# Optimization experiments

Hardware: AMD Instinct MI355X
Metric: run time of the kernel (lower is better)

## Reference

```python
import jax, jax.numpy as jnp
import numpy as np

T, D, H, E, K = 4096, 1024, 2048, 8, 2  # tokens, model dim, expert hidden, n_experts, top_k
AUX_COEF = 0.01


def setup_inputs() -> dict:
    key = jax.random.key(0)
    ks = jax.random.split(key, 8)
    sd = lambda fan_in: 1.0 / np.sqrt(fan_in)
    x = jax.random.normal(ks[0], (T, D), jnp.float32)
    Wr = jax.random.normal(ks[1], (E, D), jnp.float32) * sd(D)      # router (no bias)
    w1 = jax.random.normal(ks[2], (E, H, D), jnp.float32) * sd(D)   # stacked up-proj
    w2 = jax.random.normal(ks[3], (E, D, H), jnp.float32) * sd(H)   # stacked down-proj
    w3 = jax.random.normal(ks[4], (E, H, D), jnp.float32) * sd(D)   # stacked gate-proj
    w1s = jax.random.normal(ks[5], (H, D), jnp.float32) * sd(D)     # shared expert
    w2s = jax.random.normal(ks[6], (D, H), jnp.float32) * sd(H)
    w3s = jax.random.normal(ks[7], (H, D), jnp.float32) * sd(D)
    return dict(x=x, Wr=Wr, w1=w1, w2=w2, w3=w3, w1s=w1s, w2s=w2s, w3s=w3s)


def _gelu(v):
    return jax.nn.gelu(v, approximate=False)  # torch F.gelu default = exact erf


def reference(x, Wr, w1, w2, w3, w1s, w2s, w3s):
    n_tok = x.shape[0]
    router_out = x @ Wr.T                                   # [T, E]
    router_probs = jax.nn.softmax(router_out, axis=-1)
    _, topk_idx = jax.lax.top_k(router_out, K)              # [T, K]
    topk_probs, _ = jax.lax.top_k(router_probs, K)          # top-k of probs (same order)

    # auxiliary load-balance loss (first-choice density * mean prob)
    expert_mask = jax.nn.one_hot(topk_idx[:, 0], E, dtype=jnp.float32)
    density = expert_mask.mean(axis=0)
    aux_loss = AUX_COEF * jnp.sum(density * router_probs.mean(axis=0)) * E

    # combine weights C[t, e] = sum of routed probs for expert e at token t
    C = jnp.zeros((n_tok, E), x.dtype).at[
        jnp.arange(n_tok)[:, None], topk_idx
    ].add(topk_probs)

    # dense per-expert SwiGLU-style FFN, combined by C (equal math to
    # sort-based dispatch + scatter_add in the original)
    h = _gelu(jnp.einsum('td,ehd->teh', x, w1)) * jnp.einsum('td,ehd->teh', x, w3)
    ye = jnp.einsum('teh,edh->ted', h, w2)                  # [T, E, D]
    out = jnp.einsum('ted,te->td', ye, C)

    # shared expert (always active)
    out = out + (_gelu(x @ w1s.T) * (x @ w3s.T)) @ w2s.T
    return out, aux_loss
```

## Files before the change

kernel.cpp:

```cpp
#include <hip/hip_runtime.h>
#include <hip/hip_bf16.h>
#include <cstdint>

#define T_TOK 4096
#define DMODEL 1024
#define HDIM 2048

typedef short bf16x8 __attribute__((ext_vector_type(8)));
typedef float f32x4 __attribute__((ext_vector_type(4)));
typedef uint32_t u32x4 __attribute__((ext_vector_type(4)));

#define WAITVM(N) asm volatile("s_waitcnt vmcnt(" #N ")" ::: "memory")
#define BARX() asm volatile("s_barrier" ::: "memory")

__device__ __forceinline__ uint32_t cvt_pk_bf16(float lo, float hi) {
  uint32_t d;
  asm("v_cvt_pk_bf16_f32 %0, %1, %2" : "=v"(d) : "v"(lo), "v"(hi));
  return d;
}
__device__ __forceinline__ unsigned short f2bf(float f) {
  uint32_t d;
  asm("v_cvt_pk_bf16_f32 %0, %1, %1" : "=v"(d) : "v"(f));
  return (unsigned short)d;
}
__device__ __forceinline__ float gelu_fast(float v) {
  float z = v * 0.70710678118654752f;
  float az = fabsf(z);
  float t = __frcp_rn(1.0f + 0.3275911f * az);
  float poly = ((((1.061405429f * t - 1.453152027f) * t + 1.421413741f) * t
                 - 0.284496736f) * t + 0.254829592f) * t;
  float er = 1.0f - poly * __expf(-z * z);
  er = (z < 0.f) ? -er : er;
  return 0.5f * v * (1.0f + er);
}
__device__ __forceinline__ void gload16(const void* g, void* lds) {
  __builtin_amdgcn_global_load_lds((const __attribute__((address_space(1))) void*)g,
                                   (__attribute__((address_space(3))) void*)lds, 16, 0, 0);
}
__device__ __forceinline__ u32x4 pk8(const float* s) {
  float4 v0 = ((const float4*)s)[0], v1 = ((const float4*)s)[1];
  u32x4 p = {cvt_pk_bf16(v0.x, v0.y), cvt_pk_bf16(v0.z, v0.w),
             cvt_pk_bf16(v1.x, v1.y), cvt_pk_bf16(v1.z, v1.w)};
  return p;
}

__global__ __launch_bounds__(256) void convert_w(
    const float* __restrict__ w1, const float* __restrict__ w3,
    const float* __restrict__ w1s, const float* __restrict__ w3s,
    const float* __restrict__ w2, const float* __restrict__ w2s,
    short* __restrict__ wB, short* __restrict__ wd) {
  int bid = blockIdx.x;
  if (bid < 18432) {
    int id = bid * 256 + threadIdx.x;
    int e = id >> 19, rem = id & 524287;
    int nf = rem >> 11, k32 = (rem >> 6) & 31, ln = rem & 63;
    int h = (nf >> 1) * 16 + (ln & 15);
    size_t so = (size_t)h * DMODEL + k32 * 32 + (ln >> 4) * 8;
    const float* src = (nf & 1)
        ? ((e < 8) ? w3 + (size_t)e * 2097152 + so : w3s + so)
        : ((e < 8) ? w1 + (size_t)e * 2097152 + so : w1s + so);
    *(u32x4*)(wB + (size_t)id * 8) = pk8(src);
  } else {
    int id = (bid - 18432) * 256 + threadIdx.x;
    int e = id >> 18, rem = id & 262143;
    int d16 = rem >> 12, h32 = (rem >> 6) & 63, ln = rem & 63;
    size_t so = (size_t)(d16 * 16 + (ln & 15)) * HDIM + h32 * 32 + (ln >> 4) * 8;
    const float* s2 = (e < 8) ? w2 + (size_t)e * 2097152 + so : w2s + so;
    *(u32x4*)(wd + (size_t)id * 8) = pk8(s2);
  }
}

__global__ __launch_bounds__(256) void router_kernel(
    const float* __restrict__ x, const float* __restrict__ Wr,
    int* __restrict__ cursor, int* __restrict__ cnt1,
    float* __restrict__ psum, int* __restrict__ perm,
    int* __restrict__ tokpos, float* __restrict__ wtok,
    short* __restrict__ xb) {
  __shared__ float4 sW[8 * 256];
  __shared__ float sP[8];
  int tid = threadIdx.x;
  const float4* W4 = (const float4*)Wr;
  for (int i = tid; i < 2048; i += 256) sW[i] = W4[i];
  if (tid < 8) sP[tid] = 0.f;
  __syncthreads();

  int lane = tid & 63, wid = tid >> 6;
  int t = blockIdx.x * 4 + wid;
  float acc[8] = {0.f, 0.f, 0.f, 0.f, 0.f, 0.f, 0.f, 0.f};
  const float4* x4 = (const float4*)(x + (size_t)t * DMODEL);
#pragma unroll
  for (int it = 0; it < 4; ++it) {
    float4 xv = x4[it * 64 + lane];
    uint2 pk = {cvt_pk_bf16(xv.x, xv.y), cvt_pk_bf16(xv.z, xv.w)};
    *(uint2*)(xb + (size_t)t * DMODEL + it * 256 + lane * 4) = pk;
#pragma unroll
    for (int e = 0; e < 8; ++e) {
      float4 wv = sW[e * 256 + it * 64 + lane];
      acc[e] += xv.x * wv.x + xv.y * wv.y + xv.z * wv.z + xv.w * wv.w;
    }
  }
#pragma unroll
  for (int e = 0; e < 8; ++e)
    for (int off = 32; off; off >>= 1) acc[e] += __shfl_xor(acc[e], off);

  float mx = acc[0];
#pragma unroll
  for (int e = 1; e < 8; ++e) mx = fmaxf(mx, acc[e]);
  float ex[8], s = 0.f;
#pragma unroll
  for (int e = 0; e < 8; ++e) { ex[e] = expf(acc[e] - mx); s += ex[e]; }
  float inv = 1.f / s;
  int e0 = 0;
#pragma unroll
  for (int e = 1; e < 8; ++e) if (acc[e] > acc[e0]) e0 = e;
  int e1 = (e0 == 0) ? 1 : 0;
#pragma unroll
  for (int e = 0; e < 8; ++e) if (e != e0 && acc[e] > acc[e1]) e1 = e;

  if (lane == 0) {
#pragma unroll
    for (int e = 0; e < 8; ++e) atomicAdd(&sP[e], ex[e] * inv);
    atomicAdd(&cnt1[e0], 1);
    int s0 = atomicAdd(&cursor[e0], 1);
    perm[e0 * 4096 + s0] = t;
    int s1 = atomicAdd(&cursor[e1], 1);
    perm[e1 * 4096 + s1] = t;
    tokpos[2 * t] = (e0 << 12) | s0;
    tokpos[2 * t + 1] = (e1 << 12) | s1;
    wtok[2 * t] = ex[e0] * inv;
    wtok[2 * t + 1] = ex[e1] * inv;
  }
  __syncthreads();
  if (tid < 8) atomicAdd(&psum[tid], sP[tid]);
}

__global__ void finalize_kernel(const int* __restrict__ cursor,
                                const int* __restrict__ cnt1,
                                const float* __restrict__ psum,
                                int* __restrict__ base,
                                int* __restrict__ work256, int* __restrict__ work128,
                                int* __restrict__ n256, int* __restrict__ n128,
                                float* __restrict__ aux_out) {
  if (threadIdx.x == 0) {
    int b = 0, a = 0, c2 = 0;
    for (int e = 0; e < 9; ++e) {
      int c = (e < 8) ? cursor[e] : 4096;
      base[e] = b;
      int t2 = (c + 255) >> 8;
      for (int mt = 0; mt < t2; ++mt) work256[a++] = (e << 8) | mt;
      int t1 = (c + 127) >> 7;
      for (int mt = 0; mt < t1; ++mt) work128[c2++] = (e << 8) | mt;
      b += t2 << 8;
    }
    *n256 = a; *n128 = c2;
    float aux = 0.f;
    for (int e = 0; e < 8; ++e)
      aux += ((float)cnt1[e] * (1.f / T_TOK)) * (psum[e] * (1.f / T_TOK));
    aux_out[0] = 0.01f * 8.f * aux;
  }
}

__global__ __launch_bounds__(512) void gemm_upgate8(
    const short* __restrict__ xb, const short* __restrict__ wB,
    const int* __restrict__ cursor, const int* __restrict__ base,
    const int* __restrict__ work, const int* __restrict__ nwork,
    const int* __restrict__ perm, unsigned short* __restrict__ hbuf) {
  int y = blockIdx.y;
  if (y >= *nwork) return;
  int wk = work[y];
  int e = wk >> 8, mt = wk & 255, nt = blockIdx.x;
  int cnt = (e < 8) ? cursor[e] : 4096;
  int hb = base[e];
  const short* wE = wB + (size_t)e * 4194304;

  __shared__ short lds[65536];

  int tid = threadIdx.x, lane = tid & 63, wid = tid >> 6;
  int wm = wid >> 2, wn = wid & 3;
  int fr = lane & 15, q4r = lane >> 4;

  size_t aOff[2];
#pragma unroll
  for (int c = 0; c < 2; ++c) {
    int g = c * 8 + wid;
    int slot = mt * 256 + g * 16 + fr;
    int tok = (e == 8) ? slot : ((slot < cnt) ? perm[e * 4096 + slot] : 0);
    aOff[c] = (size_t)tok * DMODEL + q4r * 8;
  }
  size_t bOff[2];
#pragma unroll
  for (int c = 0; c < 2; ++c)
    bOff[c] = ((size_t)(nt * 16 + c * 8 + wid) * 32) * 512 + lane * 8;

  auto stageT = [&](int tt) {
    int bb = (tt & 1) * 32768;
#pragma unroll
    for (int c = 0; c < 2; ++c) {
      int g = c * 8 + wid;
#pragma unroll
      for (int k32 = 0; k32 < 2; ++k32) {
        gload16(xb + aOff[c] + tt * 64 + k32 * 32,
                &lds[bb + (k32 * 16 + g) * 512 + lane * 8]);
        gload16(wE + bOff[c] + (size_t)(tt * 2 + k32) * 512,
                &lds[bb + 16384 + (k32 * 16 + g) * 512 + lane * 8]);
      }
    }
  };

  f32x4 acc[8][4] = {};

  stageT(0);
#pragma unroll 1
  for (int t = 0; t < 16; ++t) {
    WAITVM(0);
    BARX();
    if (t < 15) stageT(t + 1);
    const short* bufp = &lds[(t & 1) * 32768];
#pragma unroll
    for (int k32 = 0; k32 < 2; ++k32) {
      bf16x8 af[8], bf[4];
#pragma unroll
      for (int i = 0; i < 8; ++i)
        af[i] = *(const bf16x8*)&bufp[(k32 * 16 + wm * 8 + i) * 512 + lane * 8];
#pragma unroll
      for (int n = 0; n < 4; ++n)
        bf[n] = *(const bf16x8*)&bufp[16384 + (k32 * 16 + wn * 4 + n) * 512 + lane * 8];
      __builtin_amdgcn_s_setprio(1);
#pragma unroll
      for (int i = 0; i < 8; ++i)
#pragma unroll
        for (int n = 0; n < 4; ++n)
          acc[i][n] = __builtin_amdgcn_mfma_f32_16x16x32_bf16(af[i], bf[n], acc[i][n], 0, 0, 0);
      __builtin_amdgcn_s_setprio(0);
    }
  }

#pragma unroll
  for (int m = 0; m < 8; ++m) {
#pragma unroll
    for (int p = 0; p < 2; ++p) {
      f32x4 u = acc[m][2 * p], g = acc[m][2 * p + 1];
      int hcol = (nt * 8 + wn * 2 + p) * 16 + fr;
#pragma unroll
      for (int j = 0; j < 4; ++j) {
        int sl = mt * 256 + wm * 128 + m * 16 + q4r * 4 + j;
        float hv = (sl < cnt) ? gelu_fast(u[j]) * g[j] : 0.f;
        hbuf[(size_t)(hb + sl) * HDIM + hcol] = f2bf(hv);
      }
    }
  }
}

__global__ __launch_bounds__(256, 2) void gemm_down(
    const unsigned short* __restrict__ hbuf,
    const short* __restrict__ wd,
    const int* __restrict__ cursor, const int* __restrict__ base,
    const int* __restrict__ work, const int* __restrict__ nwork,
    float* __restrict__ ybuf) {
  int y = blockIdx.y;
  if (y >= *nwork) return;
  int wk = work[y];
  int e = wk >> 8, mt = wk & 255, nt = blockIdx.x;
  int hb = base[e];
  const short* wdE = wd + (size_t)e * 2097152;

  __shared__ short lds[32768];

  int tid = threadIdx.x, lane = tid & 63, wid = tid >> 6;
  int fr = lane & 15, q4r = lane >> 4;
  int wr = wid >> 1, wc = wid & 1;

  size_t aOff[2], bOff[2];
#pragma unroll
  for (int c = 0; c < 2; ++c) {
    int g = c * 4 + wid;
    aOff[c] = (size_t)(hb + mt * 128 + g * 16 + fr) * HDIM + q4r * 8;
    bOff[c] = ((size_t)(nt * 8 + g) * 64) * 512 + lane * 8;
  }

  auto stageD = [&](int tt) {
    int bb = (tt & 1) * 16384;
#pragma unroll
    for (int c = 0; c < 2; ++c) {
      int g = c * 4 + wid;
#pragma unroll
      for (int k32 = 0; k32 < 2; ++k32) {
        gload16(hbuf + aOff[c] + tt * 64 + k32 * 32,
                &lds[bb + (k32 * 8 + g) * 512 + lane * 8]);
        gload16(wdE + bOff[c] + (size_t)(tt * 2 + k32) * 512,
                &lds[bb + 8192 + (k32 * 8 + g) * 512 + lane * 8]);
      }
    }
  };

  f32x4 acc[4][4] = {};

  stageD(0);
#pragma unroll 1
  for (int t = 0; t < 32; ++t) {
    WAITVM(0);
    BARX();
    if (t < 31) stageD(t + 1);
    const short* bufp = &lds[(t & 1) * 16384];
#pragma unroll
    for (int k32 = 0; k32 < 2; ++k32) {
      bf16x8 af[4], bf[4];
#pragma unroll
      for (int m = 0; m < 4; ++m)
        af[m] = *(const bf16x8*)&bufp[(k32 * 8 + wr * 4 + m) * 512 + lane * 8];
#pragma unroll
      for (int n = 0; n < 4; ++n)
        bf[n] = *(const bf16x8*)&bufp[8192 + (k32 * 8 + wc * 4 + n) * 512 + lane * 8];
      __builtin_amdgcn_s_setprio(1);
#pragma unroll
      for (int m = 0; m < 4; ++m)
#pragma unroll
        for (int n = 0; n < 4; ++n)
          acc[m][n] = __builtin_amdgcn_mfma_f32_16x16x32_bf16(af[m], bf[n], acc[m][n], 0, 0, 0);
      __builtin_amdgcn_s_setprio(0);
    }
  }

#pragma unroll
  for (int m = 0; m < 4; ++m) {
#pragma unroll
    for (int n = 0; n < 4; ++n) {
      int col = nt * 128 + wc * 64 + n * 16 + fr;
      f32x4 a = acc[m][n];
#pragma unroll
      for (int j = 0; j < 4; ++j) {
        int row = mt * 128 + wr * 64 + m * 16 + q4r * 4 + j;
        ybuf[(size_t)(hb + row) * DMODEL + col] = a[j];
      }
    }
  }
}

__global__ __launch_bounds__(256) void gather_kernel(
    const float* __restrict__ ybuf, const int* __restrict__ tokpos,
    const float* __restrict__ wtok, const int* __restrict__ base,
    float* __restrict__ out) {
  int t = blockIdx.x, c4 = threadIdx.x;
  int p0 = tokpos[2 * t], p1 = tokpos[2 * t + 1];
  float w0 = wtok[2 * t], w1 = wtok[2 * t + 1];
  size_t r0 = (size_t)(base[p0 >> 12] + (p0 & 4095)) * DMODEL;
  size_t r1 = (size_t)(base[p1 >> 12] + (p1 & 4095)) * DMODEL;
  size_t rs = (size_t)(base[8] + t) * DMODEL;
  float4 v0 = *(const float4*)(ybuf + r0 + c4 * 4);
  float4 v1 = *(const float4*)(ybuf + r1 + c4 * 4);
  float4 vs = *(const float4*)(ybuf + rs + c4 * 4);
  float4 o;
  o.x = w0 * v0.x + w1 * v1.x + vs.x;
  o.y = w0 * v0.y + w1 * v1.y + vs.y;
  o.z = w0 * v0.z + w1 * v1.z + vs.z;
  o.w = w0 * v0.w + w1 * v1.w + vs.w;
  *(float4*)(out + (size_t)t * DMODEL + c4 * 4) = o;
}

extern "C" void kernel_launch(void* const* d_in, const int* in_sizes, int n_in,
                              void* d_out, int out_size, void* d_ws, size_t ws_size,
                              hipStream_t stream) {
  const float* x   = (const float*)d_in[0];
  const float* Wr  = (const float*)d_in[1];
  const float* w1  = (const float*)d_in[2];
  const float* w2  = (const float*)d_in[3];
  const float* w3  = (const float*)d_in[4];
  const float* w1s = (const float*)d_in[5];
  const float* w2s = (const float*)d_in[6];
  const float* w3s = (const float*)d_in[7];
  float* out = (float*)d_out;

  char* ws = (char*)d_ws;
  const size_t HBUF_OFF = 0;
  const size_t XB_OFF   = 58720256;
  const size_t WB_OFF   = XB_OFF + 8388608;
  const size_t WD_OFF   = WB_OFF + 75497472;
  const size_t PERM_OFF = WD_OFF + 37748736;
  const size_t TP_OFF   = PERM_OFF + 131072;
  const size_t WT_OFF   = TP_OFF + 32768;
  const size_t CTRL_OFF = WT_OFF + 32768;
  const size_t W256_OFF = CTRL_OFF + 256;
  const size_t W128_OFF = W256_OFF + 1024;

  unsigned short* hbuf = (unsigned short*)(ws + HBUF_OFF);
  short* xb = (short*)(ws + XB_OFF);
  short* wB = (short*)(ws + WB_OFF);
  short* wd = (short*)(ws + WD_OFF);
  float* ybuf = (float*)(ws + WB_OFF);
  int*   perm   = (int*)(ws + PERM_OFF);
  int*   tokpos = (int*)(ws + TP_OFF);
  float* wtok   = (float*)(ws + WT_OFF);
  int*   cursor = (int*)(ws + CTRL_OFF);
  int*   cnt1   = (int*)(ws + CTRL_OFF + 64);
  float* psum   = (float*)(ws + CTRL_OFF + 128);
  int*   base   = (int*)(ws + CTRL_OFF + 192);
  int*   n256   = (int*)(ws + CTRL_OFF + 240);
  int*   n128   = (int*)(ws + CTRL_OFF + 244);
  int*   work256 = (int*)(ws + W256_OFF);
  int*   work128 = (int*)(ws + W128_OFF);

  hipMemsetAsync(ws + CTRL_OFF, 0, 256, stream);

  router_kernel<<<1024, 256, 0, stream>>>(x, Wr, cursor, cnt1, psum, perm,
                                          tokpos, wtok, xb);
  finalize_kernel<<<1, 64, 0, stream>>>(cursor, cnt1, psum, base,
                                        work256, work128, n256, n128,
                                        out + (size_t)T_TOK * DMODEL);
  convert_w<<<27648, 256, 0, stream>>>(w1, w3, w1s, w3s, w2, w2s, wB, wd);
  gemm_upgate8<<<dim3(16, 64), 512, 0, stream>>>(xb, wB, cursor, base,
                                                 work256, n256, perm, hbuf);
  gemm_down<<<dim3(8, 128), 256, 0, stream>>>(hbuf, wd, cursor, base,
                                              work128, n128, ybuf);
  gather_kernel<<<4096, 256, 0, stream>>>(ybuf, tokpos, wtok, base, out);
}
```

Baseline: 403.3 us.

## Interleave LDS reads, global prefetch and MFMA in grouped-GEMM main loops; enlarge down tiles

The up/gate GEMM main loop is reworked so each K step is split into quarter phases. Each phase issues part of the next tile's global-to-LDS loads, reads half the A fragments, and runs MFMAs under barriers with partial vmcnt waits, replacing a single full wait per iteration. The down-projection GEMM moves from 128x128 tiles with 256 threads to 256x256 tiles with 512 threads using the same interleaved schedule, and reuses the 256-row work list so the 128-row list is dropped. This aims to overlap memory latency with matrix math and raise operand reuse, at the cost of more barriers and higher register and LDS use per block.

After: 369.0 us. 8.5% less time.

```diff
diff --git a/kernel.cpp b/kernel.cpp
--- a/kernel.cpp
+++ b/kernel.cpp
@@ -138,21 +138,18 @@
                                 const int* __restrict__ cnt1,
                                 const float* __restrict__ psum,
                                 int* __restrict__ base,
-                                int* __restrict__ work256, int* __restrict__ work128,
-                                int* __restrict__ n256, int* __restrict__ n128,
+                                int* __restrict__ work256, int* __restrict__ n256,
                                 float* __restrict__ aux_out) {
   if (threadIdx.x == 0) {
-    int b = 0, a = 0, c2 = 0;
+    int b = 0, a = 0;
     for (int e = 0; e < 9; ++e) {
       int c = (e < 8) ? cursor[e] : 4096;
       base[e] = b;
       int t2 = (c + 255) >> 8;
       for (int mt = 0; mt < t2; ++mt) work256[a++] = (e << 8) | mt;
-      int t1 = (c + 127) >> 7;
-      for (int mt = 0; mt < t1; ++mt) work128[c2++] = (e << 8) | mt;
       b += t2 << 8;
     }
-    *n256 = a; *n128 = c2;
+    *n256 = a;
     float aux = 0.f;
     for (int e = 0; e < 8; ++e)
       aux += ((float)cnt1[e] * (1.f / T_TOK)) * (psum[e] * (1.f / T_TOK));
@@ -192,47 +189,58 @@
   for (int c = 0; c < 2; ++c)
     bOff[c] = ((size_t)(nt * 16 + c * 8 + wid) * 32) * 512 + lane * 8;
 
-  auto stageT = [&](int tt) {
-    int bb = (tt & 1) * 32768;
-#pragma unroll
-    for (int c = 0; c < 2; ++c) {
-      int g = c * 8 + wid;
-#pragma unroll
-      for (int k32 = 0; k32 < 2; ++k32) {
-        gload16(xb + aOff[c] + tt * 64 + k32 * 32,
-                &lds[bb + (k32 * 16 + g) * 512 + lane * 8]);
-        gload16(wE + bOff[c] + (size_t)(tt * 2 + k32) * 512,
-                &lds[bb + 16384 + (k32 * 16 + g) * 512 + lane * 8]);
-      }
-    }
-  };
+#define UPG_STAGE_A(tt, k32)                                                   \
+  { int bb_ = ((tt) & 1) * 32768;                                              \
+    gload16(xb + aOff[0] + (tt) * 64 + (k32) * 32,                             \
+            &lds[bb_ + ((k32) * 16 + wid) * 512 + lane * 8]);                  \
+    gload16(xb + aOff[1] + (tt) * 64 + (k32) * 32,                             \
+            &lds[bb_ + ((k32) * 16 + 8 + wid) * 512 + lane * 8]); }
+#define UPG_STAGE_B(tt, k32)                                                   \
+  { int bb_ = ((tt) & 1) * 32768;                                              \
+    gload16(wE + bOff[0] + (size_t)((tt) * 2 + (k32)) * 512,                   \
+            &lds[bb_ + 16384 + ((k32) * 16 + wid) * 512 + lane * 8]);          \
+    gload16(wE + bOff[1] + (size_t)((tt) * 2 + (k32)) * 512,                   \
+            &lds[bb_ + 16384 + ((k32) * 16 + 8 + wid) * 512 + lane * 8]); }
+#define UPG_READA(k32, mh)                                                     \
+  { _Pragma("unroll") for (int i = 0; i < 4; ++i)                              \
+      af[i] = *(const bf16x8*)&lds[bb + ((k32) * 16 + wm * 8 + (mh) * 4 + i) * \
+                                       512 + lane * 8]; }
+#define UPG_READB(k32)                                                         \
+  { _Pragma("unroll") for (int n = 0; n < 4; ++n)                              \
+      bf[n] = *(const bf16x8*)&lds[bb + 16384 + ((k32) * 16 + wn * 4 + n) *    \
+                                       512 + lane * 8]; }
+#define UPG_MFMA(mh)                                                           \
+  { __builtin_amdgcn_s_setprio(1);                                             \
+    _Pragma("unroll") for (int i = 0; i < 4; ++i)                              \
+      _Pragma("unroll") for (int n = 0; n < 4; ++n)                            \
+        acc[(mh) * 4 + i][n] = __builtin_amdgcn_mfma_f32_16x16x32_bf16(        \
+            af[i], bf[n], acc[(mh) * 4 + i][n], 0, 0, 0);                      \
+    __builtin_amdgcn_s_setprio(0); }
 
   f32x4 acc[8][4] = {};
-
-  stageT(0);
+  bf16x8 af[4], bf[4];
+
+  UPG_STAGE_A(0, 0); UPG_STAGE_B(0, 0); UPG_STAGE_A(0, 1); UPG_STAGE_B(0, 1);
+  WAITVM(4); BARX();
+
 #pragma unroll 1
-  for (int t = 0; t < 16; ++t) {
-    WAITVM(0);
-    BARX();
-    if (t < 15) stageT(t + 1);
-    const short* bufp = &lds[(t & 1) * 32768];
-#pragma unroll
-    for (int k32 = 0; k32 < 2; ++k32) {
-      bf16x8 af[8], bf[4];
-#pragma unroll
-      for (int i = 0; i < 8; ++i)
-        af[i] = *(const bf16x8*)&bufp[(k32 * 16 + wm * 8 + i) * 512 + lane * 8];
-#pragma unroll
-      for (int n = 0; n < 4; ++n)
-        bf[n] = *(const bf16x8*)&bufp[16384 + (k32 * 16 + wn * 4 + n) * 512 + lane * 8];
-      __builtin_amdgcn_s_setprio(1);
-#pragma unroll
-      for (int i = 0; i < 8; ++i)
-#pragma unroll
-        for (int n = 0; n < 4; ++n)
-          acc[i][n] = __builtin_amdgcn_mfma_f32_16x16x32_bf16(af[i], bf[n], acc[i][n], 0, 0, 0);
-      __builtin_amdgcn_s_setprio(0);
-    }
+  for (int t = 0; t < 15; ++t) {
+    const int bb = (t & 1) * 32768;
+    UPG_READA(0, 0); UPG_READB(0); UPG_STAGE_A(t + 1, 0);
+    BARX(); UPG_MFMA(0); BARX();
+    UPG_READA(0, 1); UPG_STAGE_B(t + 1, 0);
+    BARX(); UPG_MFMA(1); WAITVM(4); BARX();
+    UPG_READA(1, 0); UPG_READB(1); UPG_STAGE_A(t + 1, 1);
+    BARX(); UPG_MFMA(0); BARX();
+    UPG_READA(1, 1); UPG_STAGE_B(t + 1, 1);
+    BARX(); UPG_MFMA(1); WAITVM(4); BARX();
+  }
+  {
+    const int bb = 32768;
+    UPG_READA(0, 0); UPG_READB(0); BARX(); UPG_MFMA(0); BARX();
+    UPG_READA(0, 1); BARX(); UPG_MFMA(1); WAITVM(0); BARX();
+    UPG_READA(1, 0); UPG_READB(1); BARX(); UPG_MFMA(0); BARX();
+    UPG_READA(1, 1); UPG_MFMA(1);
   }
 
 #pragma unroll
@@ -251,10 +259,9 @@
   }
 }
 
-__global__ __launch_bounds__(256, 2) void gemm_down(
-    const unsigned short* __restrict__ hbuf,
-    const short* __restrict__ wd,
-    const int* __restrict__ cursor, const int* __restrict__ base,
+__global__ __launch_bounds__(512) void gemm_down8(
+    const unsigned short* __restrict__ hbuf, const short* __restrict__ wd,
+    const int* __restrict__ base,
     const int* __restrict__ work, const int* __restrict__ nwork,
     float* __restrict__ ybuf) {
   int y = blockIdx.y;
@@ -264,72 +271,69 @@
   int hb = base[e];
   const short* wdE = wd + (size_t)e * 2097152;
 
-  __shared__ short lds[32768];
+  __shared__ short lds[65536];
 
   int tid = threadIdx.x, lane = tid & 63, wid = tid >> 6;
+  int wm = wid >> 2, wn = wid & 3;
   int fr = lane & 15, q4r = lane >> 4;
-  int wr = wid >> 1, wc = wid & 1;
-
-  size_t aOff[2], bOff[2];
-#pragma unroll
-  for (int c = 0; c < 2; ++c) {
-    int g = c * 4 + wid;
-    aOff[c] = (size_t)(hb + mt * 128 + g * 16 + fr) * HDIM + q4r * 8;
-    bOff[c] = ((size_t)(nt * 8 + g) * 64) * 512 + lane * 8;
-  }
-
-  auto stageD = [&](int tt) {
-    int bb = (tt & 1) * 16384;
-#pragma unroll
-    for (int c = 0; c < 2; ++c) {
-      int g = c * 4 + wid;
-#pragma unroll
-      for (int k32 = 0; k32 < 2; ++k32) {
-        gload16(hbuf + aOff[c] + tt * 64 + k32 * 32,
-                &lds[bb + (k32 * 8 + g) * 512 + lane * 8]);
-        gload16(wdE + bOff[c] + (size_t)(tt * 2 + k32) * 512,
-                &lds[bb + 8192 + (k32 * 8 + g) * 512 + lane * 8]);
-      }
-    }
-  };
-
-  f32x4 acc[4][4] = {};
-
-  stageD(0);
+
+  size_t aOff[2];
+#pragma unroll
+  for (int c = 0; c < 2; ++c)
+    aOff[c] = (size_t)(hb + mt * 256 + (c * 8 + wid) * 16 + fr) * HDIM + q4r * 8;
+  size_t bOff[2];
+#pragma unroll
+  for (int c = 0; c < 2; ++c)
+    bOff[c] = ((size_t)(nt * 16 + c * 8 + wid) * 64) * 512 + lane * 8;
+
+#define DWN_STAGE_A(tt, k32)                                                   \
+  { int bb_ = ((tt) & 1) * 32768;                                              \
+    gload16(hbuf + aOff[0] + (tt) * 64 + (k32) * 32,                           \
+            &lds[bb_ + ((k32) * 16 + wid) * 512 + lane * 8]);                  \
+    gload16(hbuf + aOff[1] + (tt) * 64 + (k32) * 32,                           \
+            &lds[bb_ + ((k32) * 16 + 8 + wid) * 512 + lane * 8]); }
+#define DWN_STAGE_B(tt, k32)                                                   \
+  { int bb_ = ((tt) & 1) * 32768;                                              \
+    gload16(wdE + bOff[0] + (size_t)((tt) * 2 + (k32)) * 512,                  \
+            &lds[bb_ + 16384 + ((k32) * 16 + wid) * 512 + lane * 8]);          \
+    gload16(wdE + bOff[1] + (size_t)((tt) * 2 + (k32)) * 512,                  \
+            &lds[bb_ + 16384 + ((k32) * 16 + 8 + wid) * 512 + lane * 8]); }
+
+  f32x4 acc[8][4] = {};
+  bf16x8 af[4], bf[4];
+
+  DWN_STAGE_A(0, 0); DWN_STAGE_B(0, 0); DWN_STAGE_A(0, 1); DWN_STAGE_B(0, 1);
+  WAITVM(4); BARX();
+
 #pragma unroll 1
-  for (int t = 0; t < 32; ++t) {
-    WAITVM(0);
-    BARX();
-    if (t < 31) stageD(t + 1);
-    const short* bufp = &lds[(t & 1) * 16384];
-#pragma unroll
-    for (int k32 = 0; k32 < 2; ++k32) {
-      bf16x8 af[4], bf[4];
-#pragma unroll
-      for (int m = 0; m < 4; ++m)
-        af[m] = *(const bf16x8*)&bufp[(k32 * 8 + wr * 4 + m) * 512 + lane * 8];
-#pragma unroll
-      for (int n = 0; n < 4; ++n)
-        bf[n] = *(const bf16x8*)&bufp[8192 + (k32 * 8 + wc * 4 + n) * 512 + lane * 8];
-      __builtin_amdgcn_s_setprio(1);
-#pragma unroll
-      for (int m = 0; m < 4; ++m)
-#pragma unroll
-        for (int n = 0; n < 4; ++n)
-          acc[m][n] = __builtin_amdgcn_mfma_f32_16x16x32_bf16(af[m], bf[n], acc[m][n], 0, 0, 0);
-      __builtin_amdgcn_s_setprio(0);
-    }
-  }
-
-#pragma unroll
-  for (int m = 0; m < 4; ++m) {
+  for (int t = 0; t < 31; ++t) {
+    const int bb = (t & 1) * 32768;
+    UPG_READA(0, 0); UPG_READB(0); DWN_STAGE_A(t + 1, 0);
+    BARX(); UPG_MFMA(0); BARX();
+    UPG_READA(0, 1); DWN_STAGE_B(t + 1, 0);
+    BARX(); UPG_MFMA(1); WAITVM(4); BARX();
+    UPG_READA(1, 0); UPG_READB(1); DWN_STAGE_A(t + 1, 1);
+    BARX(); UPG_MFMA(0); BARX();
+    UPG_READA(1, 1); DWN_STAGE_B(t + 1, 1);
+    BARX(); UPG_MFMA(1); WAITVM(4); BARX();
+  }
+  {
+    const int bb = 32768;
+    UPG_READA(0, 0); UPG_READB(0); BARX(); UPG_MFMA(0); BARX();
+    UPG_READA(0, 1); BARX(); UPG_MFMA(1); WAITVM(0); BARX();
+    UPG_READA(1, 0); UPG_READB(1); BARX(); UPG_MFMA(0); BARX();
+    UPG_READA(1, 1); UPG_MFMA(1);
+  }
+
+#pragma unroll
+  for (int m = 0; m < 8; ++m) {
 #pragma unroll
     for (int n = 0; n < 4; ++n) {
-      int col = nt * 128 + wc * 64 + n * 16 + fr;
+      int col = (nt * 16 + wn * 4 + n) * 16 + fr;
       f32x4 a = acc[m][n];
 #pragma unroll
       for (int j = 0; j < 4; ++j) {
-        int row = mt * 128 + wr * 64 + m * 16 + q4r * 4 + j;
+        int row = mt * 256 + wm * 128 + m * 16 + q4r * 4 + j;
         ybuf[(size_t)(hb + row) * DMODEL + col] = a[j];
       }
     }
@@ -380,7 +384,6 @@
   const size_t WT_OFF   = TP_OFF + 32768;
   const size_t CTRL_OFF = WT_OFF + 32768;
   const size_t W256_OFF = CTRL_OFF + 256;
-  const size_t W128_OFF = W256_OFF + 1024;
 
   unsigned short* hbuf = (unsigned short*)(ws + HBUF_OFF);
   short* xb = (short*)(ws + XB_OFF);
@@ -395,21 +398,19 @@
   float* psum   = (float*)(ws + CTRL_OFF + 128);
   int*   base   = (int*)(ws + CTRL_OFF + 192);
   int*   n256   = (int*)(ws + CTRL_OFF + 240);
-  int*   n128   = (int*)(ws + CTRL_OFF + 244);
   int*   work256 = (int*)(ws + W256_OFF);
-  int*   work128 = (int*)(ws + W128_OFF);
 
   hipMemsetAsync(ws + CTRL_OFF, 0, 256, stream);
 
   router_kernel<<<1024, 256, 0, stream>>>(x, Wr, cursor, cnt1, psum, perm,
                                           tokpos, wtok, xb);
   finalize_kernel<<<1, 64, 0, stream>>>(cursor, cnt1, psum, base,
-                                        work256, work128, n256, n128,
+                                        work256, n256,
                                         out + (size_t)T_TOK * DMODEL);
   convert_w<<<27648, 256, 0, stream>>>(w1, w3, w1s, w3s, w2, w2s, wB, wd);
   gemm_upgate8<<<dim3(16, 64), 512, 0, stream>>>(xb, wB, cursor, base,
                                                  work256, n256, perm, hbuf);
-  gemm_down<<<dim3(8, 128), 256, 0, stream>>>(hbuf, wd, cursor, base,
-                                              work128, n128, ybuf);
+  gemm_down8<<<dim3(4, 64), 512, 0, stream>>>(hbuf, wd, base,
+                                              work256, n256, ybuf);
   gather_kernel<<<4096, 256, 0, stream>>>(ybuf, tokpos, wtok, base, out);
 }
```

## Shrink up-gate GEMM tiles to 128x128, flatten grids with XCD-aware block remap

Applied to the files above, without the earlier changes.

The up/gate GEMM goes from 256-row, 512-thread blocks with 64-wide K steps to 128-row, 256-thread blocks with 32-wide K steps. That cuts LDS use and allows three blocks per CU. Expert padding drops from 256 to 128 rows, and a single work list is shared by both GEMMs. Both GEMMs now launch a flat 1D grid, remapped so neighbouring tiles land on the same XCD for L2 reuse. The costs are more blocks, more barriers from the smaller K steps, and less reuse per block of the loaded A/B tiles.

After: 405.8 us. No clear change (+0.6%).

```diff
diff --git a/kernel.cpp b/kernel.cpp
--- a/kernel.cpp
+++ b/kernel.cpp
@@ -9,9 +9,6 @@
 typedef short bf16x8 __attribute__((ext_vector_type(8)));
 typedef float f32x4 __attribute__((ext_vector_type(4)));
 typedef uint32_t u32x4 __attribute__((ext_vector_type(4)));
-
-#define WAITVM(N) asm volatile("s_waitcnt vmcnt(" #N ")" ::: "memory")
-#define BARX() asm volatile("s_barrier" ::: "memory")
 
 __device__ __forceinline__ uint32_t cvt_pk_bf16(float lo, float hi) {
   uint32_t d;
@@ -42,6 +39,10 @@
   u32x4 p = {cvt_pk_bf16(v0.x, v0.y), cvt_pk_bf16(v0.z, v0.w),
              cvt_pk_bf16(v1.x, v1.y), cvt_pk_bf16(v1.z, v1.w)};
   return p;
+}
+__device__ __forceinline__ int xcd_remap(int d, int nblk) {
+  int q = nblk >> 3, r = nblk & 7, xc = d & 7, i = d >> 3;
+  return (xc < r ? xc * (q + 1) : r * (q + 1) + (xc - r) * q) + i;
 }
 
 __global__ __launch_bounds__(256) void convert_w(
@@ -138,21 +139,18 @@
                                 const int* __restrict__ cnt1,
                                 const float* __restrict__ psum,
                                 int* __restrict__ base,
-                                int* __restrict__ work256, int* __restrict__ work128,
-                                int* __restrict__ n256, int* __restrict__ n128,
+                                int* __restrict__ work, int* __restrict__ nwork,
                                 float* __restrict__ aux_out) {
   if (threadIdx.x == 0) {
-    int b = 0, a = 0, c2 = 0;
+    int b = 0, a = 0;
     for (int e = 0; e < 9; ++e) {
       int c = (e < 8) ? cursor[e] : 4096;
       base[e] = b;
-      int t2 = (c + 255) >> 8;
-      for (int mt = 0; mt < t2; ++mt) work256[a++] = (e << 8) | mt;
       int t1 = (c + 127) >> 7;
-      for (int mt = 0; mt < t1; ++mt) work128[c2++] = (e << 8) | mt;
-      b += t2 << 8;
-    }
-    *n256 = a; *n128 = c2;
+      for (int mt = 0; mt < t1; ++mt) work[a++] = (e << 8) | mt;
+      b += t1 << 7;
+    }
+    *nwork = a;
     float aux = 0.f;
     for (int e = 0; e < 8; ++e)
       aux += ((float)cnt1[e] * (1.f / T_TOK)) * (psum[e] * (1.f / T_TOK));
@@ -160,90 +158,87 @@
   }
 }
 
-__global__ __launch_bounds__(512) void gemm_upgate8(
+__global__ __launch_bounds__(256, 3) void gemm_upgate(
     const short* __restrict__ xb, const short* __restrict__ wB,
     const int* __restrict__ cursor, const int* __restrict__ base,
     const int* __restrict__ work, const int* __restrict__ nwork,
     const int* __restrict__ perm, unsigned short* __restrict__ hbuf) {
-  int y = blockIdx.y;
-  if (y >= *nwork) return;
+  int nblk = *nwork * 32;
+  int d = blockIdx.x;
+  if (d >= nblk) return;
+  int o = xcd_remap(d, nblk);
+  int y = o >> 5, nt = o & 31;
   int wk = work[y];
-  int e = wk >> 8, mt = wk & 255, nt = blockIdx.x;
+  int e = wk >> 8, mt = wk & 255;
   int cnt = (e < 8) ? cursor[e] : 4096;
   int hb = base[e];
   const short* wE = wB + (size_t)e * 4194304;
 
-  __shared__ short lds[65536];
+  __shared__ short lds[16384];
 
   int tid = threadIdx.x, lane = tid & 63, wid = tid >> 6;
-  int wm = wid >> 2, wn = wid & 3;
   int fr = lane & 15, q4r = lane >> 4;
-
-  size_t aOff[2];
+  int wm = wid >> 1, wn = wid & 1;
+
+  size_t aOff[2], bOff[2];
 #pragma unroll
   for (int c = 0; c < 2; ++c) {
-    int g = c * 8 + wid;
-    int slot = mt * 256 + g * 16 + fr;
+    int g = c * 4 + wid;
+    int slot = mt * 128 + g * 16 + fr;
     int tok = (e == 8) ? slot : ((slot < cnt) ? perm[e * 4096 + slot] : 0);
     aOff[c] = (size_t)tok * DMODEL + q4r * 8;
-  }
-  size_t bOff[2];
-#pragma unroll
-  for (int c = 0; c < 2; ++c)
-    bOff[c] = ((size_t)(nt * 16 + c * 8 + wid) * 32) * 512 + lane * 8;
-
-  auto stageT = [&](int tt) {
-    int bb = (tt & 1) * 32768;
+    bOff[c] = (size_t)(nt * 8 + g) * 32 * 512 + lane * 8;
+  }
+
+  auto stage = [&](int b, int t) {
 #pragma unroll
     for (int c = 0; c < 2; ++c) {
-      int g = c * 8 + wid;
-#pragma unroll
-      for (int k32 = 0; k32 < 2; ++k32) {
-        gload16(xb + aOff[c] + tt * 64 + k32 * 32,
-                &lds[bb + (k32 * 16 + g) * 512 + lane * 8]);
-        gload16(wE + bOff[c] + (size_t)(tt * 2 + k32) * 512,
-                &lds[bb + 16384 + (k32 * 16 + g) * 512 + lane * 8]);
-      }
+      int g = c * 4 + wid;
+      gload16(xb + aOff[c] + t * 32, &lds[b * 8192 + g * 512 + lane * 8]);
+      gload16(wE + bOff[c] + (size_t)t * 512,
+              &lds[b * 8192 + 4096 + g * 512 + lane * 8]);
     }
   };
 
-  f32x4 acc[8][4] = {};
-
-  stageT(0);
+  f32x4 acc[4][4] = {};
+
+  auto compute = [&](int b) {
+    bf16x8 af[4], bf[4];
+#pragma unroll
+    for (int m = 0; m < 4; ++m)
+      af[m] = *(const bf16x8*)&lds[b * 8192 + (wm * 4 + m) * 512 + lane * 8];
+#pragma unroll
+    for (int n = 0; n < 4; ++n)
+      bf[n] = *(const bf16x8*)&lds[b * 8192 + 4096 + (wn * 4 + n) * 512 + lane * 8];
+    __builtin_amdgcn_s_setprio(1);
+#pragma unroll
+    for (int m = 0; m < 4; ++m)
+#pragma unroll
+      for (int n = 0; n < 4; ++n)
+        acc[m][n] = __builtin_amdgcn_mfma_f32_16x16x32_bf16(af[m], bf[n], acc[m][n], 0, 0, 0);
+    __builtin_amdgcn_s_setprio(0);
+  };
+
+  stage(0, 0);
+  __syncthreads();
+  int b = 0;
 #pragma unroll 1
-  for (int t = 0; t < 16; ++t) {
-    WAITVM(0);
-    BARX();
-    if (t < 15) stageT(t + 1);
-    const short* bufp = &lds[(t & 1) * 32768];
-#pragma unroll
-    for (int k32 = 0; k32 < 2; ++k32) {
-      bf16x8 af[8], bf[4];
-#pragma unroll
-      for (int i = 0; i < 8; ++i)
-        af[i] = *(const bf16x8*)&bufp[(k32 * 16 + wm * 8 + i) * 512 + lane * 8];
-#pragma unroll
-      for (int n = 0; n < 4; ++n)
-        bf[n] = *(const bf16x8*)&bufp[16384 + (k32 * 16 + wn * 4 + n) * 512 + lane * 8];
-      __builtin_amdgcn_s_setprio(1);
-#pragma unroll
-      for (int i = 0; i < 8; ++i)
-#pragma unroll
-        for (int n = 0; n < 4; ++n)
-          acc[i][n] = __builtin_amdgcn_mfma_f32_16x16x32_bf16(af[i], bf[n], acc[i][n], 0, 0, 0);
-      __builtin_amdgcn_s_setprio(0);
-    }
-  }
-
-#pragma unroll
-  for (int m = 0; m < 8; ++m) {
+  for (int t = 0; t < 32; ++t) {
+    if (t < 31) stage(b ^ 1, t + 1);
+    compute(b);
+    __syncthreads();
+    b ^= 1;
+  }
+
+#pragma unroll
+  for (int m = 0; m < 4; ++m) {
 #pragma unroll
     for (int p = 0; p < 2; ++p) {
       f32x4 u = acc[m][2 * p], g = acc[m][2 * p + 1];
-      int hcol = (nt * 8 + wn * 2 + p) * 16 + fr;
+      int hcol = (nt * 4 + wn * 2 + p) * 16 + fr;
 #pragma unroll
       for (int j = 0; j < 4; ++j) {
-        int sl = mt * 256 + wm * 128 + m * 16 + q4r * 4 + j;
+        int sl = mt * 128 + wm * 64 + m * 16 + q4r * 4 + j;
         float hv = (sl < cnt) ? gelu_fast(u[j]) * g[j] : 0.f;
         hbuf[(size_t)(hb + sl) * HDIM + hcol] = f2bf(hv);
       }
@@ -251,85 +246,84 @@
   }
 }
 
-__global__ __launch_bounds__(256, 2) void gemm_down(
-    const unsigned short* __restrict__ hbuf,
-    const short* __restrict__ wd,
-    const int* __restrict__ cursor, const int* __restrict__ base,
+__global__ __launch_bounds__(256, 3) void gemm_down(
+    const unsigned short* __restrict__ hbuf, const short* __restrict__ wd,
+    const int* __restrict__ base,
     const int* __restrict__ work, const int* __restrict__ nwork,
     float* __restrict__ ybuf) {
-  int y = blockIdx.y;
-  if (y >= *nwork) return;
+  int nblk = *nwork * 8;
+  int d = blockIdx.x;
+  if (d >= nblk) return;
+  int o = xcd_remap(d, nblk);
+  int y = o >> 3, nt = o & 7;
   int wk = work[y];
-  int e = wk >> 8, mt = wk & 255, nt = blockIdx.x;
+  int e = wk >> 8, mt = wk & 255;
   int hb = base[e];
   const short* wdE = wd + (size_t)e * 2097152;
 
-  __shared__ short lds[32768];
+  __shared__ short lds[16384];
 
   int tid = threadIdx.x, lane = tid & 63, wid = tid >> 6;
   int fr = lane & 15, q4r = lane >> 4;
-  int wr = wid >> 1, wc = wid & 1;
+  int wm = wid >> 1, wn = wid & 1;
 
   size_t aOff[2], bOff[2];
 #pragma unroll
   for (int c = 0; c < 2; ++c) {
     int g = c * 4 + wid;
     aOff[c] = (size_t)(hb + mt * 128 + g * 16 + fr) * HDIM + q4r * 8;
-    bOff[c] = ((size_t)(nt * 8 + g) * 64) * 512 + lane * 8;
-  }
-
-  auto stageD = [&](int tt) {
-    int bb = (tt & 1) * 16384;
+    bOff[c] = (size_t)(nt * 8 + g) * 64 * 512 + lane * 8;
+  }
+
+  auto stage = [&](int b, int t) {
 #pragma unroll
     for (int c = 0; c < 2; ++c) {
       int g = c * 4 + wid;
-#pragma unroll
-      for (int k32 = 0; k32 < 2; ++k32) {
-        gload16(hbuf + aOff[c] + tt * 64 + k32 * 32,
-                &lds[bb + (k32 * 8 + g) * 512 + lane * 8]);
-        gload16(wdE + bOff[c] + (size_t)(tt * 2 + k32) * 512,
-                &lds[bb + 8192 + (k32 * 8 + g) * 512 + lane * 8]);
-      }
+      gload16(hbuf + aOff[c] + t * 32, &lds[b * 8192 + g * 512 + lane * 8]);
+      gload16(wdE + bOff[c] + (size_t)t * 512,
+              &lds[b * 8192 + 4096 + g * 512 + lane * 8]);
     }
   };
 
   f32x4 acc[4][4] = {};
 
-  stageD(0);
+  auto compute = [&](int b) {
+    bf16x8 af[4], bf[4];
+#pragma unroll
+    for (int m = 0; m < 4; ++m)
+      af[m] = *(const bf16x8*)&lds[b * 8192 + (wm * 4 + m) * 512 + lane * 8];
+#pragma unroll
+    for (int n = 0; n < 4; ++n)
+      bf[n] = *(const bf16x8*)&lds[b * 8192 + 4096 + (wn * 4 + n) * 512 + lane * 8];
+    __builtin_amdgcn_s_setprio(1);
+#pragma unroll
+    for (int m = 0; m < 4; ++m)
+#pragma unroll
+      for (int n = 0; n < 4; ++n)
+        acc[m][n] = __builtin_amdgcn_mfma_f32_16x16x32_bf16(af[m], bf[n], acc[m][n], 0, 0, 0);
+    __builtin_amdgcn_s_setprio(0);
+  };
+
+  stage(0, 0);
+  __syncthreads();
+  int b = 0;
 #pragma unroll 1
-  for (int t = 0; t < 32; ++t) {
-    WAITVM(0);
-    BARX();
-    if (t < 31) stageD(t + 1);
-    const short* bufp = &lds[(t & 1) * 16384];
-#pragma unroll
-    for (int k32 = 0; k32 < 2; ++k32) {
-      bf16x8 af[4], bf[4];
-#pragma unroll
-      for (int m = 0; m < 4; ++m)
-        af[m] = *(const bf16x8*)&bufp[(k32 * 8 + wr * 4 + m) * 512 + lane * 8];
-#pragma unroll
-      for (int n = 0; n < 4; ++n)
-        bf[n] = *(const bf16x8*)&bufp[8192 + (k32 * 8 + wc * 4 + n) * 512 + lane * 8];
-      __builtin_amdgcn_s_setprio(1);
-#pragma unroll
-      for (int m = 0; m < 4; ++m)
-#pragma unroll
-        for (int n = 0; n < 4; ++n)
-          acc[m][n] = __builtin_amdgcn_mfma_f32_16x16x32_bf16(af[m], bf[n], acc[m][n], 0, 0, 0);
-      __builtin_amdgcn_s_setprio(0);
-    }
+  for (int t = 0; t < 64; ++t) {
+    if (t < 63) stage(b ^ 1, t + 1);
+    compute(b);
+    __syncthreads();
+    b ^= 1;
   }
 
 #pragma unroll
   for (int m = 0; m < 4; ++m) {
 #pragma unroll
     for (int n = 0; n < 4; ++n) {
-      int col = nt * 128 + wc * 64 + n * 16 + fr;
+      int col = (nt * 8 + wn * 4 + n) * 16 + fr;
       f32x4 a = acc[m][n];
 #pragma unroll
       for (int j = 0; j < 4; ++j) {
-        int row = mt * 128 + wr * 64 + m * 16 + q4r * 4 + j;
+        int row = mt * 128 + wm * 64 + m * 16 + q4r * 4 + j;
         ybuf[(size_t)(hb + row) * DMODEL + col] = a[j];
       }
     }
@@ -379,8 +373,7 @@
   const size_t TP_OFF   = PERM_OFF + 131072;
   const size_t WT_OFF   = TP_OFF + 32768;
   const size_t CTRL_OFF = WT_OFF + 32768;
-  const size_t W256_OFF = CTRL_OFF + 256;
-  const size_t W128_OFF = W256_OFF + 1024;
+  const size_t WORK_OFF = CTRL_OFF + 256;
 
   unsigned short* hbuf = (unsigned short*)(ws + HBUF_OFF);
   short* xb = (short*)(ws + XB_OFF);
@@ -394,22 +387,18 @@
   int*   cnt1   = (int*)(ws + CTRL_OFF + 64);
   float* psum   = (float*)(ws + CTRL_OFF + 128);
   int*   base   = (int*)(ws + CTRL_OFF + 192);
-  int*   n256   = (int*)(ws + CTRL_OFF + 240);
-  int*   n128   = (int*)(ws + CTRL_OFF + 244);
-  int*   work256 = (int*)(ws + W256_OFF);
-  int*   work128 = (int*)(ws + W128_OFF);
+  int*   nwork  = (int*)(ws + CTRL_OFF + 240);
+  int*   work   = (int*)(ws + WORK_OFF);
 
   hipMemsetAsync(ws + CTRL_OFF, 0, 256, stream);
 
   router_kernel<<<1024, 256, 0, stream>>>(x, Wr, cursor, cnt1, psum, perm,
                                           tokpos, wtok, xb);
-  finalize_kernel<<<1, 64, 0, stream>>>(cursor, cnt1, psum, base,
-                                        work256, work128, n256, n128,
+  finalize_kernel<<<1, 64, 0, stream>>>(cursor, cnt1, psum, base, work, nwork,
                                         out + (size_t)T_TOK * DMODEL);
   convert_w<<<27648, 256, 0, stream>>>(w1, w3, w1s, w3s, w2, w2s, wB, wd);
-  gemm_upgate8<<<dim3(16, 64), 512, 0, stream>>>(xb, wB, cursor, base,
-                                                 work256, n256, perm, hbuf);
-  gemm_down<<<dim3(8, 128), 256, 0, stream>>>(hbuf, wd, cursor, base,
-                                              work128, n128, ybuf);
+  gemm_upgate<<<3328, 256, 0, stream>>>(xb, wB, cursor, base, work, nwork,
+                                        perm, hbuf);
+  gemm_down<<<832, 256, 0, stream>>>(hbuf, wd, base, work, nwork, ybuf);
   gather_kernel<<<4096, 256, 0, stream>>>(ybuf, tokpos, wtok, base, out);
 }
```
